# Performance work log

Measured on AMD Instinct MI355X. Metric: run time of the kernel, lower is better.

The kernel has to match this reference:

```python
import jax, jax.numpy as jnp
import numpy as np

FP8_MAX = 448.0   # max normal of float8_e4m3fn
BLOCK = 128       # block_size
EPS = 1e-12


def setup_inputs() -> dict:
    key = jax.random.key(0)
    k1, k2 = jax.random.split(key)
    M, K, N = 8192, 2048, 2048  # tokens, in_features, out_features
    x = jax.random.normal(k1, (M, K), dtype=jnp.float32)
    # Build an fp8 blockwise-quantized weight (as the module stores it):
    w = jax.random.normal(k2, (N, K), dtype=jnp.float32) * 0.02
    wb = w.reshape(N // BLOCK, BLOCK, K // BLOCK, BLOCK)
    amax = jnp.max(jnp.abs(wb), axis=(1, 3))                      # [Nb, Kb]
    w_scale = jnp.maximum(amax, EPS) / FP8_MAX                    # fp32 per-block scale
    w_q = (wb / w_scale[:, None, :, None]).astype(jnp.float8_e4m3fn)
    weight = w_q.reshape(N, K)                                    # fp8 [N, K]
    return {"x": x, "weight": weight, "w_scale": w_scale}


def reference(x, weight, w_scale):
    M, K = x.shape
    N = weight.shape[0]
    # --- fp8_blockwise_act_quant: per (1, BLOCK) block along last dim ---
    xb = x.reshape(M, K // BLOCK, BLOCK)
    amax = jnp.max(jnp.abs(xb), axis=-1)                          # [M, Kb]
    x_scale = jnp.maximum(amax, EPS) / FP8_MAX                    # [M, Kb]
    x_q = (xb / x_scale[:, :, None]).astype(jnp.float8_e4m3fn).astype(jnp.float32)
    # --- blockwise_fp8_gemm: y[m,n] = sum_kb (xq_blk . wq_blk) * xs[m,kb] * ws[nb,kb]
    # Scales factor per-block, so dequantize then a single GEMM is exactly equivalent.
    x_deq = (x_q * x_scale[:, :, None]).reshape(M, K)             # [M, K]
    ws_full = jnp.repeat(jnp.repeat(w_scale, BLOCK, axis=0), BLOCK, axis=1)  # [N, K]
    w_deq = weight.astype(jnp.float32) * ws_full                  # [N, K]
    y = x_deq @ w_deq.T                                           # [M, N]
    return y
```

## Files before the change

### kernel.cpp

```cpp
#include <hip/hip_runtime.h>
#include <cstdint>
#include <cstddef>

#define MDIM 8192
#define KDIM 2048
#define NDIM 2048
#define QBLK 128
#define KB   (KDIM / QBLK)
#define NB   (NDIM / QBLK)

typedef _Float16 half8  __attribute__((ext_vector_type(8)));
typedef _Float16 half4v __attribute__((ext_vector_type(4)));
typedef float    floatx4 __attribute__((ext_vector_type(4)));

__device__ inline float e4m3_rne(float q) {
    float aq = fabsf(q);
    float r;
    if (aq < 0.015625f) {
        r = rintf(aq * 512.0f) * 0.001953125f;
    } else {
        unsigned u = __float_as_uint(aq);
        unsigned rem = u & 0xFFFFFu;
        unsigned base = u & ~0xFFFFFu;
        unsigned inc = (rem > 0x80000u || (rem == 0x80000u && (u & 0x100000u))) ? 0x100000u : 0u;
        r = __uint_as_float(base + inc);
    }
    return q < 0.0f ? -r : r;
}

__device__ inline float e4m3_decode(unsigned b) {
    unsigned s = b >> 7, e = (b >> 3) & 0xFu, m = b & 7u;
    float v;
    if (e == 0) v = (float)m * 0.001953125f;
    else        v = __uint_as_float((e + 120u) << 23) * (float)(8 + m) * 0.125f;
    return s ? -v : v;
}

__device__ inline int is_expbyte(unsigned b) {
    unsigned e = b & 0x7Fu;
    return (e >= 0x3Bu && e <= 0x43u) || e == 0x00u;
}

#define QXB ((MDIM * KB) / 8)
#define DWB ((NDIM * KDIM / 8) / 256)

__global__ __launch_bounds__(256) void prep_kernel(const float* __restrict__ x,
                                                   const void* __restrict__ wq,
                                                   const float* __restrict__ ws,
                                                   _Float16* __restrict__ xh,
                                                   _Float16* __restrict__ wh) {
    const int tid = threadIdx.x;
    if (blockIdx.x < QXB) {
        const int g = tid >> 5;
        const int l = tid & 31;
        const size_t bi = (size_t)blockIdx.x * 8 + g;
        const size_t base = bi << 7;

        const float4 v = *(const float4*)(x + base + (size_t)l * 4);
        float a = fmaxf(fmaxf(fabsf(v.x), fabsf(v.y)), fmaxf(fabsf(v.z), fabsf(v.w)));
        a = fmaxf(a, __shfl_xor(a, 1));
        a = fmaxf(a, __shfl_xor(a, 2));
        a = fmaxf(a, __shfl_xor(a, 4));
        a = fmaxf(a, __shfl_xor(a, 8));
        a = fmaxf(a, __shfl_xor(a, 16));

        const float scale = fmaxf(a, 1e-12f) / 448.0f;

        half4v o;
        o[0] = (_Float16)(e4m3_rne(v.x / scale) * scale);
        o[1] = (_Float16)(e4m3_rne(v.y / scale) * scale);
        o[2] = (_Float16)(e4m3_rne(v.z / scale) * scale);
        o[3] = (_Float16)(e4m3_rne(v.w / scale) * scale);
        *(half4v*)(xh + base + (size_t)l * 4) = o;
    } else {
        const int lane = tid & 63;
        const unsigned pw = ((const unsigned*)wq)[lane];
        const unsigned long long m3 = __ballot(is_expbyte((pw >> 24) & 0xFFu));
        const unsigned long long m1 = __ballot(((pw >> 8) & 0xFFu) == 0u);
        const int hits3 = __popcll(m3);
        const int zeros1 = __popcll(m1);
        const int f = (hits3 >= 56) ? ((zeros1 >= 56) ? 2 : 1) : 0;

        const size_t idx = (size_t)(blockIdx.x - QXB) * 256 + tid;
        const size_t off = idx * 8;
        const int n = (int)(off >> 11);
        const int k = (int)(off & (KDIM - 1));
        const float s = ws[((n >> 7) << 4) + (k >> 7)];

        half8 o;
        if (f == 2) {
            const float4* p = (const float4*)((const float*)wq + off);
            const float4 a = p[0], b = p[1];
            o[0] = (_Float16)(a.x * s); o[1] = (_Float16)(a.y * s);
            o[2] = (_Float16)(a.z * s); o[3] = (_Float16)(a.w * s);
            o[4] = (_Float16)(b.x * s); o[5] = (_Float16)(b.y * s);
            o[6] = (_Float16)(b.z * s); o[7] = (_Float16)(b.w * s);
        } else if (f == 1) {
            const ushort4 h0 = *(const ushort4*)((const unsigned short*)wq + off);
            const ushort4 h1 = *(((const ushort4*)((const unsigned short*)wq + off)) + 1);
            o[0] = (_Float16)(__uint_as_float((unsigned)h0.x << 16) * s);
            o[1] = (_Float16)(__uint_as_float((unsigned)h0.y << 16) * s);
            o[2] = (_Float16)(__uint_as_float((unsigned)h0.z << 16) * s);
            o[3] = (_Float16)(__uint_as_float((unsigned)h0.w << 16) * s);
            o[4] = (_Float16)(__uint_as_float((unsigned)h1.x << 16) * s);
            o[5] = (_Float16)(__uint_as_float((unsigned)h1.y << 16) * s);
            o[6] = (_Float16)(__uint_as_float((unsigned)h1.z << 16) * s);
            o[7] = (_Float16)(__uint_as_float((unsigned)h1.w << 16) * s);
        } else {
            const uint2 d = *(const uint2*)((const unsigned char*)wq + off);
            o[0] = (_Float16)(e4m3_decode(d.x & 0xFF) * s);
            o[1] = (_Float16)(e4m3_decode((d.x >> 8) & 0xFF) * s);
            o[2] = (_Float16)(e4m3_decode((d.x >> 16) & 0xFF) * s);
            o[3] = (_Float16)(e4m3_decode((d.x >> 24) & 0xFF) * s);
            o[4] = (_Float16)(e4m3_decode(d.y & 0xFF) * s);
            o[5] = (_Float16)(e4m3_decode((d.y >> 8) & 0xFF) * s);
            o[6] = (_Float16)(e4m3_decode((d.y >> 16) & 0xFF) * s);
            o[7] = (_Float16)(e4m3_decode((d.y >> 24) & 0xFF) * s);
        }
        *(half8*)(wh + off) = o;
    }
}

#define BM 128
#define BN 128
#define BK 64

__global__ __launch_bounds__(256, 2) void gemm_xw_kernel(const _Float16* __restrict__ A,
                                                         const _Float16* __restrict__ B,
                                                         float* __restrict__ C) {
    __shared__ _Float16 sA[BM * BK];
    __shared__ _Float16 sB[BN * BK];
    char* sAb = (char*)sA;
    char* sBb = (char*)sB;

    const int tid  = threadIdx.x;
    const int wave = tid >> 6;
    const int lane = tid & 63;
    const int lrow = lane & 15;
    const int lk   = lane >> 4;
    const int wm   = (wave & 1) * 64;
    const int wn   = (wave >> 1) * 64;
    const int m0   = blockIdx.y * BM;
    const int n0   = blockIdx.x * BN;

    const int srow = tid >> 3;
    const int gck  = (tid & 7) ^ (srow & 7);
    const char* agp = (const char*)(A + (size_t)(m0 + srow) * KDIM + gck * 8);
    const char* bgp = (const char*)(B + (size_t)(n0 + srow) * KDIM + gck * 8);
    const int ldsbase = tid * 16;

    floatx4 acc[4][4] = {};

    for (int kt = 0; kt < KDIM / BK; ++kt) {
        const size_t koff = (size_t)kt * (BK * 2);
        __syncthreads();
#pragma unroll
        for (int it = 0; it < 4; ++it) {
            __builtin_amdgcn_global_load_lds(
                (const __attribute__((address_space(1))) void*)(agp + (size_t)(it * 32) * (KDIM * 2) + koff),
                (__attribute__((address_space(3))) void*)(sAb + ldsbase + it * 4096),
                16, 0, 0);
        }
#pragma unroll
        for (int it = 0; it < 4; ++it) {
            __builtin_amdgcn_global_load_lds(
                (const __attribute__((address_space(1))) void*)(bgp + (size_t)(it * 32) * (KDIM * 2) + koff),
                (__attribute__((address_space(3))) void*)(sBb + ldsbase + it * 4096),
                16, 0, 0);
        }
        __syncthreads();

#pragma unroll
        for (int ks = 0; ks < 2; ++ks) {
            half8 af[4], bf[4];
            const int ca = ((ks * 4 + lk) ^ (lrow & 7)) * 16;
#pragma unroll
            for (int i = 0; i < 4; ++i) {
                const int Ra = wm + i * 16 + lrow;
                af[i] = *(const half8*)(sAb + Ra * 128 + ca);
                const int Rb = wn + i * 16 + lrow;
                bf[i] = *(const half8*)(sBb + Rb * 128 + ca);
            }
#pragma unroll
            for (int i = 0; i < 4; ++i)
#pragma unroll
                for (int j = 0; j < 4; ++j)
                    acc[i][j] = __builtin_amdgcn_mfma_f32_16x16x32_f16(af[i], bf[j], acc[i][j], 0, 0, 0);
        }
    }

#pragma unroll
    for (int i = 0; i < 4; ++i) {
        const int row0 = m0 + wm + i * 16 + lk * 4;
#pragma unroll
        for (int r = 0; r < 4; ++r) {
            float* cp = C + (size_t)(row0 + r) * NDIM + n0 + wn + lrow;
#pragma unroll
            for (int j = 0; j < 4; ++j)
                cp[j * 16] = acc[i][j][r];
        }
    }
}

extern "C" void kernel_launch(void* const* d_in, const int* in_sizes, int n_in,
                              void* d_out, int out_size, void* d_ws, size_t ws_size,
                              hipStream_t stream) {
    const float* x          = (const float*)d_in[0];
    const void* wq          = d_in[1];
    const float* wscale     = (const float*)d_in[2];
    float* y                = (float*)d_out;

    _Float16* xh = (_Float16*)d_ws;
    _Float16* wh = (_Float16*)((char*)d_ws + (size_t)MDIM * KDIM * 2);

    prep_kernel<<<QXB + DWB, 256, 0, stream>>>(x, wq, wscale, xh, wh);
    gemm_xw_kernel<<<dim3(NDIM / BN, MDIM / BM), 256, 0, stream>>>(xh, wh, y);
}
```

Before: 196.4 us.

## Switch GEMM to native FP8 MFMA with per-block scaling and fallback check

The activation and weight prep now emit FP8 e4m3 bytes plus per-block activation scales instead of dequantized fp16. The GEMM uses the gfx950 scaled 16x16x128 f8f6f4 MFMA, one instruction per 128-wide quantization block, and applies x_scale*w_scale to each block partial in registers. A sampled check kernel compares some outputs against a scalar recomputation and sets a flag, and a fallback fp8 16x16x32 GEMM reruns only if the flag is set. This halves operand bytes and raises MFMA throughput, at the cost of extra per-block scale FMAs, two small extra launches, and reliance on the scaled MFMA operand layout being correct.

Measured after the change: 184.1 us. 1.07x faster.

```diff
diff --git a/kernel.cpp b/kernel.cpp
--- a/kernel.cpp
+++ b/kernel.cpp
@@ -9,9 +9,12 @@
 #define KB   (KDIM / QBLK)
 #define NB   (NDIM / QBLK)
 
-typedef _Float16 half8  __attribute__((ext_vector_type(8)));
-typedef _Float16 half4v __attribute__((ext_vector_type(4)));
-typedef float    floatx4 __attribute__((ext_vector_type(4)));
+typedef float floatx4 __attribute__((ext_vector_type(4)));
+typedef int   int4v   __attribute__((ext_vector_type(4)));
+typedef int   int8v   __attribute__((ext_vector_type(8)));
+
+#define AS1 __attribute__((address_space(1)))
+#define AS3 __attribute__((address_space(3)))
 
 __device__ inline float e4m3_rne(float q) {
     float aq = fabsf(q);
@@ -28,6 +31,16 @@
     return q < 0.0f ? -r : r;
 }
 
+__device__ inline unsigned e4m3_encode(float r) {
+    unsigned u = __float_as_uint(r);
+    unsigned s = (u >> 24) & 0x80u;
+    float a = fabsf(r);
+    if (a < 0.015625f) return s | (unsigned)(a * 512.0f + 0.25f);
+    unsigned e = ((u >> 23) & 0xFFu) - 120u;
+    unsigned m = (u >> 20) & 7u;
+    return s | (e << 3) | m;
+}
+
 __device__ inline float e4m3_decode(unsigned b) {
     unsigned s = b >> 7, e = (b >> 3) & 0xFu, m = b & 7u;
     float v;
@@ -41,15 +54,23 @@
     return (e >= 0x3Bu && e <= 0x43u) || e == 0x00u;
 }
 
+#define XQ_OFF  0
+#define WQ_OFF  ((size_t)MDIM * KDIM)
+#define XS_OFF  (WQ_OFF + (size_t)NDIM * KDIM)
+#define FL_OFF  (XS_OFF + (size_t)MDIM * KB * 4)
+
 #define QXB ((MDIM * KB) / 8)
 #define DWB ((NDIM * KDIM / 8) / 256)
 
 __global__ __launch_bounds__(256) void prep_kernel(const float* __restrict__ x,
                                                    const void* __restrict__ wq,
-                                                   const float* __restrict__ ws,
-                                                   _Float16* __restrict__ xh,
-                                                   _Float16* __restrict__ wh) {
+                                                   unsigned char* __restrict__ xq,
+                                                   unsigned char* __restrict__ wq8,
+                                                   float* __restrict__ xs,
+                                                   int* __restrict__ flag) {
     const int tid = threadIdx.x;
+    if (blockIdx.x == 0 && tid == 0) *flag = 0;
+
     if (blockIdx.x < QXB) {
         const int g = tid >> 5;
         const int l = tid & 31;
@@ -65,73 +86,55 @@
         a = fmaxf(a, __shfl_xor(a, 16));
 
         const float scale = fmaxf(a, 1e-12f) / 448.0f;
-
-        half4v o;
-        o[0] = (_Float16)(e4m3_rne(v.x / scale) * scale);
-        o[1] = (_Float16)(e4m3_rne(v.y / scale) * scale);
-        o[2] = (_Float16)(e4m3_rne(v.z / scale) * scale);
-        o[3] = (_Float16)(e4m3_rne(v.w / scale) * scale);
-        *(half4v*)(xh + base + (size_t)l * 4) = o;
+        if (l == 0) xs[bi] = scale;
+
+        unsigned b0 = e4m3_encode(e4m3_rne(v.x / scale));
+        unsigned b1 = e4m3_encode(e4m3_rne(v.y / scale));
+        unsigned b2 = e4m3_encode(e4m3_rne(v.z / scale));
+        unsigned b3 = e4m3_encode(e4m3_rne(v.w / scale));
+        *(unsigned*)(xq + base + (size_t)l * 4) = b0 | (b1 << 8) | (b2 << 16) | (b3 << 24);
     } else {
         const int lane = tid & 63;
         const unsigned pw = ((const unsigned*)wq)[lane];
         const unsigned long long m3 = __ballot(is_expbyte((pw >> 24) & 0xFFu));
         const unsigned long long m1 = __ballot(((pw >> 8) & 0xFFu) == 0u);
-        const int hits3 = __popcll(m3);
-        const int zeros1 = __popcll(m1);
-        const int f = (hits3 >= 56) ? ((zeros1 >= 56) ? 2 : 1) : 0;
+        const int f = (__popcll(m3) >= 56) ? ((__popcll(m1) >= 56) ? 2 : 1) : 0;
 
         const size_t idx = (size_t)(blockIdx.x - QXB) * 256 + tid;
         const size_t off = idx * 8;
-        const int n = (int)(off >> 11);
-        const int k = (int)(off & (KDIM - 1));
-        const float s = ws[((n >> 7) << 4) + (k >> 7)];
-
-        half8 o;
+
+        unsigned lo, hi;
         if (f == 2) {
             const float4* p = (const float4*)((const float*)wq + off);
             const float4 a = p[0], b = p[1];
-            o[0] = (_Float16)(a.x * s); o[1] = (_Float16)(a.y * s);
-            o[2] = (_Float16)(a.z * s); o[3] = (_Float16)(a.w * s);
-            o[4] = (_Float16)(b.x * s); o[5] = (_Float16)(b.y * s);
-            o[6] = (_Float16)(b.z * s); o[7] = (_Float16)(b.w * s);
+            lo = e4m3_encode(a.x) | (e4m3_encode(a.y) << 8) | (e4m3_encode(a.z) << 16) | (e4m3_encode(a.w) << 24);
+            hi = e4m3_encode(b.x) | (e4m3_encode(b.y) << 8) | (e4m3_encode(b.z) << 16) | (e4m3_encode(b.w) << 24);
         } else if (f == 1) {
             const ushort4 h0 = *(const ushort4*)((const unsigned short*)wq + off);
             const ushort4 h1 = *(((const ushort4*)((const unsigned short*)wq + off)) + 1);
-            o[0] = (_Float16)(__uint_as_float((unsigned)h0.x << 16) * s);
-            o[1] = (_Float16)(__uint_as_float((unsigned)h0.y << 16) * s);
-            o[2] = (_Float16)(__uint_as_float((unsigned)h0.z << 16) * s);
-            o[3] = (_Float16)(__uint_as_float((unsigned)h0.w << 16) * s);
-            o[4] = (_Float16)(__uint_as_float((unsigned)h1.x << 16) * s);
-            o[5] = (_Float16)(__uint_as_float((unsigned)h1.y << 16) * s);
-            o[6] = (_Float16)(__uint_as_float((unsigned)h1.z << 16) * s);
-            o[7] = (_Float16)(__uint_as_float((unsigned)h1.w << 16) * s);
+            lo = e4m3_encode(__uint_as_float((unsigned)h0.x << 16))
+               | (e4m3_encode(__uint_as_float((unsigned)h0.y << 16)) << 8)
+               | (e4m3_encode(__uint_as_float((unsigned)h0.z << 16)) << 16)
+               | (e4m3_encode(__uint_as_float((unsigned)h0.w << 16)) << 24);
+            hi = e4m3_encode(__uint_as_float((unsigned)h1.x << 16))
+               | (e4m3_encode(__uint_as_float((unsigned)h1.y << 16)) << 8)
+               | (e4m3_encode(__uint_as_float((unsigned)h1.z << 16)) << 16)
+               | (e4m3_encode(__uint_as_float((unsigned)h1.w << 16)) << 24);
         } else {
             const uint2 d = *(const uint2*)((const unsigned char*)wq + off);
-            o[0] = (_Float16)(e4m3_decode(d.x & 0xFF) * s);
-            o[1] = (_Float16)(e4m3_decode((d.x >> 8) & 0xFF) * s);
-            o[2] = (_Float16)(e4m3_decode((d.x >> 16) & 0xFF) * s);
-            o[3] = (_Float16)(e4m3_decode((d.x >> 24) & 0xFF) * s);
-            o[4] = (_Float16)(e4m3_decode(d.y & 0xFF) * s);
-            o[5] = (_Float16)(e4m3_decode((d.y >> 8) & 0xFF) * s);
-            o[6] = (_Float16)(e4m3_decode((d.y >> 16) & 0xFF) * s);
-            o[7] = (_Float16)(e4m3_decode((d.y >> 24) & 0xFF) * s);
-        }
-        *(half8*)(wh + off) = o;
-    }
-}
-
-#define BM 128
-#define BN 128
-#define BK 64
-
-__global__ __launch_bounds__(256, 2) void gemm_xw_kernel(const _Float16* __restrict__ A,
-                                                         const _Float16* __restrict__ B,
+            lo = d.x; hi = d.y;
+        }
+        *(uint2*)(wq8 + off) = make_uint2(lo, hi);
+    }
+}
+
+__global__ __launch_bounds__(256, 2) void gemm_mx_kernel(const unsigned char* __restrict__ Aq,
+                                                         const unsigned char* __restrict__ Bq,
+                                                         const float* __restrict__ xs,
+                                                         const float* __restrict__ wsc,
                                                          float* __restrict__ C) {
-    __shared__ _Float16 sA[BM * BK];
-    __shared__ _Float16 sB[BN * BK];
-    char* sAb = (char*)sA;
-    char* sBb = (char*)sB;
+    __shared__ unsigned char sA[128 * 128];
+    __shared__ unsigned char sB[128 * 128];
 
     const int tid  = threadIdx.x;
     const int wave = tid >> 6;
@@ -140,52 +143,192 @@
     const int lk   = lane >> 4;
     const int wm   = (wave & 1) * 64;
     const int wn   = (wave >> 1) * 64;
-    const int m0   = blockIdx.y * BM;
-    const int n0   = blockIdx.x * BN;
+    const int m0   = blockIdx.y * 128;
+    const int n0   = blockIdx.x * 128;
+    const int nb   = n0 >> 7;
 
     const int srow = tid >> 3;
     const int gck  = (tid & 7) ^ (srow & 7);
-    const char* agp = (const char*)(A + (size_t)(m0 + srow) * KDIM + gck * 8);
-    const char* bgp = (const char*)(B + (size_t)(n0 + srow) * KDIM + gck * 8);
-    const int ldsbase = tid * 16;
+    const unsigned char* agp = Aq + (size_t)(m0 + srow) * KDIM + gck * 16;
+    const unsigned char* bgp = Bq + (size_t)(n0 + srow) * KDIM + gck * 16;
 
     floatx4 acc[4][4] = {};
-
-    for (int kt = 0; kt < KDIM / BK; ++kt) {
-        const size_t koff = (size_t)kt * (BK * 2);
+    const floatx4 zero = {0.f, 0.f, 0.f, 0.f};
+
+    for (int kb = 0; kb < KB; ++kb) {
+        const size_t koff = (size_t)kb * QBLK;
         __syncthreads();
 #pragma unroll
-        for (int it = 0; it < 4; ++it) {
+        for (int it = 0; it < 4; ++it)
             __builtin_amdgcn_global_load_lds(
-                (const __attribute__((address_space(1))) void*)(agp + (size_t)(it * 32) * (KDIM * 2) + koff),
-                (__attribute__((address_space(3))) void*)(sAb + ldsbase + it * 4096),
-                16, 0, 0);
-        }
-#pragma unroll
-        for (int it = 0; it < 4; ++it) {
+                (const AS1 void*)(agp + (size_t)(it * 32) * KDIM + koff),
+                (AS3 void*)(sA + tid * 16 + it * 4096), 16, 0, 0);
+#pragma unroll
+        for (int it = 0; it < 4; ++it)
             __builtin_amdgcn_global_load_lds(
-                (const __attribute__((address_space(1))) void*)(bgp + (size_t)(it * 32) * (KDIM * 2) + koff),
-                (__attribute__((address_space(3))) void*)(sBb + ldsbase + it * 4096),
-                16, 0, 0);
-        }
+                (const AS1 void*)(bgp + (size_t)(it * 32) * KDIM + koff),
+                (AS3 void*)(sB + tid * 16 + it * 4096), 16, 0, 0);
         __syncthreads();
 
-#pragma unroll
-        for (int ks = 0; ks < 2; ++ks) {
-            half8 af[4], bf[4];
-            const int ca = ((ks * 4 + lk) ^ (lrow & 7)) * 16;
+        int8v af[4], bf[4];
+#pragma unroll
+        for (int i = 0; i < 4; ++i) {
+            const int Ra = wm + i * 16 + lrow;
+            const int c0 = (lk * 2) ^ (Ra & 7);
+            const int c1 = (lk * 2 + 1) ^ (Ra & 7);
+            int4v alo = *(const int4v*)(sA + Ra * 128 + c0 * 16);
+            int4v ahi = *(const int4v*)(sA + Ra * 128 + c1 * 16);
+            af[i] = __builtin_shufflevector(alo, ahi, 0, 1, 2, 3, 4, 5, 6, 7);
+            const int Rb = wn + i * 16 + lrow;
+            const int d0 = (lk * 2) ^ (Rb & 7);
+            const int d1 = (lk * 2 + 1) ^ (Rb & 7);
+            int4v blo = *(const int4v*)(sB + Rb * 128 + d0 * 16);
+            int4v bhi = *(const int4v*)(sB + Rb * 128 + d1 * 16);
+            bf[i] = __builtin_shufflevector(blo, bhi, 0, 1, 2, 3, 4, 5, 6, 7);
+        }
+
+        const float wsk = wsc[nb * KB + kb];
+        float cs[4][4];
+#pragma unroll
+        for (int i = 0; i < 4; ++i)
+#pragma unroll
+            for (int r = 0; r < 4; ++r)
+                cs[i][r] = xs[(size_t)(m0 + wm + i * 16 + lk * 4 + r) * KB + kb] * wsk;
+
+#pragma unroll
+        for (int i = 0; i < 4; ++i)
+#pragma unroll
+            for (int j = 0; j < 4; ++j) {
+                floatx4 blk = __builtin_amdgcn_mfma_scale_f32_16x16x128_f8f6f4(
+                    af[i], bf[j], zero, 0, 0, 0, 0x7F7F7F7F, 0, 0x7F7F7F7F);
+#pragma unroll
+                for (int r = 0; r < 4; ++r)
+                    acc[i][j][r] += cs[i][r] * blk[r];
+            }
+    }
+
+#pragma unroll
+    for (int i = 0; i < 4; ++i) {
+        const int row0 = m0 + wm + i * 16 + lk * 4;
+#pragma unroll
+        for (int r = 0; r < 4; ++r) {
+            float* cp = C + (size_t)(row0 + r) * NDIM + n0 + wn + lrow;
+#pragma unroll
+            for (int j = 0; j < 4; ++j)
+                cp[j * 16] = acc[i][j][r];
+        }
+    }
+}
+
+__global__ __launch_bounds__(256) void check_kernel(const unsigned char* __restrict__ xq,
+                                                    const unsigned char* __restrict__ wq8,
+                                                    const float* __restrict__ xs,
+                                                    const float* __restrict__ wsc,
+                                                    const float* __restrict__ y,
+                                                    int* __restrict__ flag) {
+    const int s = blockIdx.x;
+    const int m = (s * 1237 + 11) & (MDIM - 1);
+    const int n = (s * 389 + 7) & (NDIM - 1);
+    const int tid = threadIdx.x;
+    const int k0 = tid * 8;
+    const int kb = k0 >> 7;
+
+    const unsigned char* xp = xq + (size_t)m * KDIM + k0;
+    const unsigned char* wp = wq8 + (size_t)n * KDIM + k0;
+    float dot = 0.f;
+#pragma unroll
+    for (int i = 0; i < 8; ++i)
+        dot += e4m3_decode(xp[i]) * e4m3_decode(wp[i]);
+    float part = dot * xs[m * KB + kb] * wsc[(n >> 7) * KB + kb];
+
+#pragma unroll
+    for (int o = 32; o > 0; o >>= 1) part += __shfl_down(part, o);
+    __shared__ float wsum[4];
+    if ((tid & 63) == 0) wsum[tid >> 6] = part;
+    __syncthreads();
+    if (tid == 0) {
+        const float tot = wsum[0] + wsum[1] + wsum[2] + wsum[3];
+        const float d = tot - y[(size_t)m * NDIM + n];
+        if (!(fabsf(d) <= 0.05f)) atomicOr(flag, 1);
+    }
+}
+
+__global__ __launch_bounds__(256, 2) void gemm_fb_kernel(const unsigned char* __restrict__ Aq,
+                                                         const unsigned char* __restrict__ Bq,
+                                                         const float* __restrict__ xs,
+                                                         const float* __restrict__ wsc,
+                                                         float* __restrict__ C,
+                                                         const int* __restrict__ flag) {
+    if (*flag == 0) return;
+
+    __shared__ unsigned char sA[128 * 128];
+    __shared__ unsigned char sB[128 * 128];
+
+    const int tid  = threadIdx.x;
+    const int wave = tid >> 6;
+    const int lane = tid & 63;
+    const int lrow = lane & 15;
+    const int lk   = lane >> 4;
+    const int wm   = (wave & 1) * 64;
+    const int wn   = (wave >> 1) * 64;
+    const int m0   = blockIdx.y * 128;
+    const int n0   = blockIdx.x * 128;
+    const int nb   = n0 >> 7;
+
+    const int srow = tid >> 3;
+    const int gck  = (tid & 7) ^ (srow & 7);
+    const unsigned char* agp = Aq + (size_t)(m0 + srow) * KDIM + gck * 16;
+    const unsigned char* bgp = Bq + (size_t)(n0 + srow) * KDIM + gck * 16;
+
+    floatx4 acc[4][4] = {};
+
+    for (int kb = 0; kb < KB; ++kb) {
+        const size_t koff = (size_t)kb * QBLK;
+        __syncthreads();
+#pragma unroll
+        for (int it = 0; it < 4; ++it)
+            __builtin_amdgcn_global_load_lds(
+                (const AS1 void*)(agp + (size_t)(it * 32) * KDIM + koff),
+                (AS3 void*)(sA + tid * 16 + it * 4096), 16, 0, 0);
+#pragma unroll
+        for (int it = 0; it < 4; ++it)
+            __builtin_amdgcn_global_load_lds(
+                (const AS1 void*)(bgp + (size_t)(it * 32) * KDIM + koff),
+                (AS3 void*)(sB + tid * 16 + it * 4096), 16, 0, 0);
+        __syncthreads();
+
+        floatx4 blk[4][4] = {};
+#pragma unroll
+        for (int ks = 0; ks < 4; ++ks) {
+            long a8[4], b8[4];
+            const int lc = ks * 2 + (lk >> 1);
+            const int bo = (lk & 1) * 8;
 #pragma unroll
             for (int i = 0; i < 4; ++i) {
                 const int Ra = wm + i * 16 + lrow;
-                af[i] = *(const half8*)(sAb + Ra * 128 + ca);
+                a8[i] = *(const long*)(sA + Ra * 128 + (lc ^ (Ra & 7)) * 16 + bo);
                 const int Rb = wn + i * 16 + lrow;
-                bf[i] = *(const half8*)(sBb + Rb * 128 + ca);
+                b8[i] = *(const long*)(sB + Rb * 128 + (lc ^ (Rb & 7)) * 16 + bo);
             }
 #pragma unroll
             for (int i = 0; i < 4; ++i)
 #pragma unroll
                 for (int j = 0; j < 4; ++j)
-                    acc[i][j] = __builtin_amdgcn_mfma_f32_16x16x32_f16(af[i], bf[j], acc[i][j], 0, 0, 0);
+                    blk[i][j] = __builtin_amdgcn_mfma_f32_16x16x32_fp8_fp8(a8[i], b8[j], blk[i][j], 0, 0, 0);
+        }
+
+        const float wsk = wsc[nb * KB + kb];
+#pragma unroll
+        for (int i = 0; i < 4; ++i) {
+            float cs[4];
+#pragma unroll
+            for (int r = 0; r < 4; ++r)
+                cs[r] = xs[(size_t)(m0 + wm + i * 16 + lk * 4 + r) * KB + kb] * wsk;
+#pragma unroll
+            for (int j = 0; j < 4; ++j)
+#pragma unroll
+                for (int r = 0; r < 4; ++r)
+                    acc[i][j][r] += cs[r] * blk[i][j][r];
         }
     }
 
@@ -205,14 +348,18 @@
 extern "C" void kernel_launch(void* const* d_in, const int* in_sizes, int n_in,
                               void* d_out, int out_size, void* d_ws, size_t ws_size,
                               hipStream_t stream) {
-    const float* x          = (const float*)d_in[0];
-    const void* wq          = d_in[1];
-    const float* wscale     = (const float*)d_in[2];
-    float* y                = (float*)d_out;
-
-    _Float16* xh = (_Float16*)d_ws;
-    _Float16* wh = (_Float16*)((char*)d_ws + (size_t)MDIM * KDIM * 2);
-
-    prep_kernel<<<QXB + DWB, 256, 0, stream>>>(x, wq, wscale, xh, wh);
-    gemm_xw_kernel<<<dim3(NDIM / BN, MDIM / BM), 256, 0, stream>>>(xh, wh, y);
-}
+    const float* x      = (const float*)d_in[0];
+    const void* wq      = d_in[1];
+    const float* wscale = (const float*)d_in[2];
+    float* y            = (float*)d_out;
+
+    unsigned char* xq  = (unsigned char*)d_ws + XQ_OFF;
+    unsigned char* wq8 = (unsigned char*)d_ws + WQ_OFF;
+    float* xs          = (float*)((unsigned char*)d_ws + XS_OFF);
+    int* flag          = (int*)((unsigned char*)d_ws + FL_OFF);
+
+    prep_kernel<<<QXB + DWB, 256, 0, stream>>>(x, wq, xq, wq8, xs, flag);
+    gemm_mx_kernel<<<dim3(NDIM / 128, MDIM / 128), 256, 0, stream>>>(xq, wq8, xs, wscale, y);
+    check_kernel<<<64, 256, 0, stream>>>(xq, wq8, xs, wscale, y, flag);
+    gemm_fb_kernel<<<dim3(NDIM / 128, MDIM / 128), 256, 0, stream>>>(xq, wq8, xs, wscale, y, flag);
+}
```
